# Performance work log

Measured on AMD Instinct MI355X. Metric: run time of the kernel, lower is better.

## Reference

```python
import jax, jax.numpy as jnp
import numpy as np

N, S, H = 16, 2048, 1024
K = 8           # num_models (experts)
D = H // 4      # bottleneck = hidden_dim // ds_factor


def setup_inputs() -> dict:
    key = jax.random.key(0)
    k1, k2, k3, k4, k5, k6 = jax.random.split(key, 6)
    hidden_states = jax.random.normal(k1, (N, S, H), dtype=jnp.float32)
    p = jax.random.uniform(k2, (N, K), dtype=jnp.float32)
    prob = p / jnp.sum(p, axis=-1, keepdims=True)  # normalized routing probs
    std = 0.02
    w_down = jax.random.normal(k3, (K, D, H), dtype=jnp.float32) * std
    b_down = jax.random.normal(k4, (K, D), dtype=jnp.float32) * std
    w_up = jax.random.normal(k5, (K, H, D), dtype=jnp.float32) * std
    b_up = jax.random.normal(k6, (K, H), dtype=jnp.float32) * std
    return {"hidden_states": hidden_states, "prob": prob,
            "w_down": w_down, "b_down": b_down,
            "w_up": w_up, "b_up": b_up}


def merge_linear(x, prob, weight, bias):
    # weight: (K, out, in); prob: (N, K) -> per-instance merged weight (N, out, in)
    w = jnp.einsum('nk,koi->noi', prob, weight)
    b = jnp.einsum('nk,ko->no', prob, bias)
    # x: (N, S, in) -> (N, S, out); matmul with per-instance weight^T
    y = jnp.einsum('nsi,noi->nso', x, w)
    return y + b[:, None, :]


def reference(hidden_states, prob, w_down, b_down, w_up, b_up):
    # MergeAdapter forward (ln_before=False, ln_after=False, dropout=0)
    residual = merge_linear(hidden_states, prob, w_down, b_down)
    residual = jax.nn.relu(residual)
    residual = merge_linear(residual, prob, w_up, b_up)
    return hidden_states + residual
```

## Files before the change

kernel.cpp:

```cpp
#include <hip/hip_runtime.h>


typedef unsigned short u16;
typedef __bf16 bf16x8 __attribute__((ext_vector_type(8)));
typedef float f32x4 __attribute__((ext_vector_type(4)));

__device__ __forceinline__ u16 f2bf(float f) {
    union { float f; unsigned int i; } v; v.f = f;
    unsigned int r = v.i + 0x7fffu + ((v.i >> 16) & 1u);
    return (u16)(r >> 16);
}

__device__ __forceinline__ void gload_lds16(const u16* g, u16* l) {
    __builtin_amdgcn_global_load_lds(
        (const __attribute__((address_space(1))) void*)g,
        (__attribute__((address_space(3))) void*)l,
        16, 0, 0);
}

__global__ __launch_bounds__(256)
void merge_kernel(const float* __restrict__ prob,
                  const float* __restrict__ w_down, const float* __restrict__ b_down,
                  const float* __restrict__ w_up,   const float* __restrict__ b_up,
                  u16* __restrict__ Wd, u16* __restrict__ Wu,
                  float* __restrict__ bd, float* __restrict__ bu)
{
    __shared__ float sp[128];
    const int tid = threadIdx.x;
    if (tid < 128) sp[tid] = prob[tid];
    __syncthreads();

    const int bid = blockIdx.x;
    const int E = 256 * 1024;

    if (bid < 256) {
        int v = bid * 256 + tid;
        const bool down = (v < 32768);
        const int vv = down ? v : (v - 32768);
        const float* W = down ? w_down : w_up;
        u16* O = down ? Wd : Wu;
        const size_t e = (size_t)vv * 8;

        float wf[8][8];
        #pragma unroll
        for (int k = 0; k < 8; ++k) {
            const float4 f0 = *(const float4*)(W + (size_t)k * E + e);
            const float4 f1 = *(const float4*)(W + (size_t)k * E + e + 4);
            wf[k][0] = f0.x; wf[k][1] = f0.y; wf[k][2] = f0.z; wf[k][3] = f0.w;
            wf[k][4] = f1.x; wf[k][5] = f1.y; wf[k][6] = f1.z; wf[k][7] = f1.w;
        }
        for (int n = 0; n < 16; ++n) {
            float a[8] = {0.f,0.f,0.f,0.f,0.f,0.f,0.f,0.f};
            #pragma unroll
            for (int k = 0; k < 8; ++k) {
                const float p = sp[n * 8 + k];
                #pragma unroll
                for (int j = 0; j < 8; ++j) a[j] = fmaf(p, wf[k][j], a[j]);
            }
            union { uint4 u; u16 s[8]; } ov;
            #pragma unroll
            for (int j = 0; j < 8; ++j) ov.s[j] = f2bf(a[j]);
            *(uint4*)(O + (size_t)n * E + e) = ov.u;
        }
    } else {
        int idx = (bid - 256) * 256 + tid;
        if (idx < 16 * 256) {
            const int n = idx >> 8, d = idx & 255;
            float s = 0.f;
            #pragma unroll
            for (int k = 0; k < 8; ++k)
                s = fmaf(sp[n * 8 + k], b_down[k * 256 + d], s);
            bd[idx] = s;
        } else {
            const int i2 = idx - 4096;
            const int n = i2 >> 10, h = i2 & 1023;
            float s = 0.f;
            #pragma unroll
            for (int k = 0; k < 8; ++k)
                s = fmaf(sp[n * 8 + k], b_up[k * 1024 + h], s);
            bu[i2] = s;
        }
    }
}

__global__ __launch_bounds__(256, 2)
void gemm_down(const float* __restrict__ A, const u16* __restrict__ B,
               const float* __restrict__ bias, u16* __restrict__ C,
               int M, int Nn, int K)
{
    __shared__ __align__(16) u16 As[128 * 64];
    __shared__ __align__(16) u16 Bs[128 * 64];

    const int batch = blockIdx.z;
    A += (size_t)batch * M * K;
    B += (size_t)batch * Nn * K;
    bias += (size_t)batch * Nn;
    C += (size_t)batch * M * Nn;

    const int tid = threadIdx.x;
    const int lane = tid & 63;
    const int wave = tid >> 6;
    const int wm = wave >> 1, wn = wave & 1;
    const int quad = lane >> 4, rl = lane & 15;
    const int tm = blockIdx.y, tn = blockIdx.x;

    const float* Ag = A + (size_t)tm * 128 * K;
    const u16* Bg = B + (size_t)tn * 128 * K;

    f32x4 acc[4][4] = {};

    for (int k0 = 0; k0 < K; k0 += 64) {
        #pragma unroll
        for (int r = 0; r < 4; ++r) {
            const int li = r * 256 + tid;
            const int row = li >> 3;
            const int col = (li & 7) * 8;
            const int ldsbase = (r * 256 + (tid & 192)) * 8;
            gload_lds16(Bg + (size_t)row * K + (k0 + col), &Bs[ldsbase]);
        }
        #pragma unroll
        for (int r = 0; r < 4; ++r) {
            const int li = r * 256 + tid;
            const int row = li >> 3;
            const int col = (li & 7) * 8;
            const float4 f0 = *(const float4*)(Ag + (size_t)row * K + (k0 + col));
            const float4 f1 = *(const float4*)(Ag + (size_t)row * K + (k0 + col) + 4);
            union { uint4 u; u16 s[8]; } cv;
            cv.s[0] = f2bf(f0.x); cv.s[1] = f2bf(f0.y);
            cv.s[2] = f2bf(f0.z); cv.s[3] = f2bf(f0.w);
            cv.s[4] = f2bf(f1.x); cv.s[5] = f2bf(f1.y);
            cv.s[6] = f2bf(f1.z); cv.s[7] = f2bf(f1.w);
            *(uint4*)(As + (size_t)li * 8) = cv.u;
        }
        __syncthreads();

        #pragma unroll
        for (int kk = 0; kk < 64; kk += 32) {
            bf16x8 af[4], bfr[4];
            #pragma unroll
            for (int mi = 0; mi < 4; ++mi)
                af[mi] = *(const bf16x8*)(As + (wm * 64 + mi * 16 + rl) * 64 + kk + quad * 8);
            #pragma unroll
            for (int ni = 0; ni < 4; ++ni)
                bfr[ni] = *(const bf16x8*)(Bs + (wn * 64 + ni * 16 + rl) * 64 + kk + quad * 8);
            #pragma unroll
            for (int mi = 0; mi < 4; ++mi)
                #pragma unroll
                for (int ni = 0; ni < 4; ++ni)
                    acc[mi][ni] = __builtin_amdgcn_mfma_f32_16x16x32_bf16(
                        af[mi], bfr[ni], acc[mi][ni], 0, 0, 0);
        }
        __syncthreads();
    }

    #pragma unroll
    for (int ni = 0; ni < 4; ++ni) {
        const int col = tn * 128 + wn * 64 + ni * 16 + rl;
        const float bv = bias[col];
        #pragma unroll
        for (int mi = 0; mi < 4; ++mi) {
            #pragma unroll
            for (int i = 0; i < 4; ++i) {
                const int row = tm * 128 + wm * 64 + mi * 16 + quad * 4 + i;
                float v = fmaxf(acc[mi][ni][i] + bv, 0.0f);
                C[(size_t)row * Nn + col] = f2bf(v);
            }
        }
    }
}

__global__ __launch_bounds__(256, 2)
void gemm_up(const u16* __restrict__ A, const u16* __restrict__ B,
             const float* __restrict__ bias, const float* __restrict__ Res,
             float* __restrict__ C, int M, int Nn, int K)
{
    __shared__ __align__(16) u16 As[128 * 64];
    __shared__ __align__(16) u16 Bs[128 * 64];

    const int batch = blockIdx.z;
    A += (size_t)batch * M * K;
    B += (size_t)batch * Nn * K;
    bias += (size_t)batch * Nn;
    Res += (size_t)batch * M * Nn;
    C += (size_t)batch * M * Nn;

    const int tid = threadIdx.x;
    const int lane = tid & 63;
    const int wave = tid >> 6;
    const int wm = wave >> 1, wn = wave & 1;
    const int quad = lane >> 4, rl = lane & 15;
    const int tm = blockIdx.y, tn = blockIdx.x;

    const u16* Ag = A + (size_t)tm * 128 * K;
    const u16* Bg = B + (size_t)tn * 128 * K;

    f32x4 acc[4][4] = {};

    for (int k0 = 0; k0 < K; k0 += 64) {
        #pragma unroll
        for (int r = 0; r < 4; ++r) {
            const int li = r * 256 + tid;
            const int row = li >> 3;
            const int col = (li & 7) * 8;
            const int ldsbase = (r * 256 + (tid & 192)) * 8;
            gload_lds16(Ag + (size_t)row * K + (k0 + col), &As[ldsbase]);
        }
        #pragma unroll
        for (int r = 0; r < 4; ++r) {
            const int li = r * 256 + tid;
            const int row = li >> 3;
            const int col = (li & 7) * 8;
            const int ldsbase = (r * 256 + (tid & 192)) * 8;
            gload_lds16(Bg + (size_t)row * K + (k0 + col), &Bs[ldsbase]);
        }
        __syncthreads();

        #pragma unroll
        for (int kk = 0; kk < 64; kk += 32) {
            bf16x8 af[4], bfr[4];
            #pragma unroll
            for (int mi = 0; mi < 4; ++mi)
                af[mi] = *(const bf16x8*)(As + (wm * 64 + mi * 16 + rl) * 64 + kk + quad * 8);
            #pragma unroll
            for (int ni = 0; ni < 4; ++ni)
                bfr[ni] = *(const bf16x8*)(Bs + (wn * 64 + ni * 16 + rl) * 64 + kk + quad * 8);
            #pragma unroll
            for (int mi = 0; mi < 4; ++mi)
                #pragma unroll
                for (int ni = 0; ni < 4; ++ni)
                    acc[mi][ni] = __builtin_amdgcn_mfma_f32_16x16x32_bf16(
                        af[mi], bfr[ni], acc[mi][ni], 0, 0, 0);
        }
        __syncthreads();
    }

    #pragma unroll
    for (int ni = 0; ni < 4; ++ni) {
        const int col = tn * 128 + wn * 64 + ni * 16 + rl;
        const float bv = bias[col];
        #pragma unroll
        for (int mi = 0; mi < 4; ++mi) {
            #pragma unroll
            for (int i = 0; i < 4; ++i) {
                const int row = tm * 128 + wm * 64 + mi * 16 + quad * 4 + i;
                const size_t off = (size_t)row * Nn + col;
                C[off] = acc[mi][ni][i] + bv + Res[off];
            }
        }
    }
}

extern "C" void kernel_launch(void* const* d_in, const int* in_sizes, int n_in,
                              void* d_out, int out_size, void* d_ws, size_t ws_size,
                              hipStream_t stream) {
    const float* hidden = (const float*)d_in[0];
    const float* prob   = (const float*)d_in[1];
    const float* w_down = (const float*)d_in[2];
    const float* b_down = (const float*)d_in[3];
    const float* w_up   = (const float*)d_in[4];
    const float* b_up   = (const float*)d_in[5];
    float* out = (float*)d_out;

    u16* Wd = (u16*)d_ws;
    u16* Wu = Wd + (size_t)16 * 256 * 1024;
    u16* R  = Wu + (size_t)16 * 1024 * 256;
    float* bd = (float*)(R + (size_t)16 * 2048 * 256);
    float* bu = bd + 16 * 256;

    merge_kernel<<<336, 256, 0, stream>>>(prob, w_down, b_down, w_up, b_up,
                                          Wd, Wu, bd, bu);

    gemm_down<<<dim3(2, 16, 16), 256, 0, stream>>>(
        hidden, Wd, bd, R, 2048, 256, 1024);

    gemm_up<<<dim3(8, 16, 16), 256, 0, stream>>>(
        R, Wu, bu, hidden, out, 2048, 1024, 256);
}
```

Baseline: 337.5 us.

## Fuse down and up projection GEMMs into one kernel with LDS-resident intermediate

Replaces the separate down-projection and up-projection GEMM kernels with one fused kernel. Each 512-thread block computes a 128-row tile of the ReLU bottleneck into LDS and then runs the up-projection over eight 128-column chunks, adding bias and the residual. This removes the global round trip of the intermediate activation and one launch. In exchange the grid shrinks to 256 large blocks at one block per CU, the up phase has no load/compute overlap, and x is read twice.

```diff
diff --git a/kernel.cpp b/kernel.cpp
--- a/kernel.cpp
+++ b/kernel.cpp
@@ -83,168 +83,135 @@
     }
 }
 
-__global__ __launch_bounds__(256, 2)
-void gemm_down(const float* __restrict__ A, const u16* __restrict__ B,
-               const float* __restrict__ bias, u16* __restrict__ C,
-               int M, int Nn, int K)
+__global__ __launch_bounds__(512, 1)
+void fused_adapter(const float* __restrict__ x, const u16* __restrict__ Wd,
+                   const u16* __restrict__ Wu, const float* __restrict__ bd,
+                   const float* __restrict__ bu, float* __restrict__ out)
 {
-    __shared__ __align__(16) u16 As[128 * 64];
-    __shared__ __align__(16) u16 Bs[128 * 64];
-
-    const int batch = blockIdx.z;
-    A += (size_t)batch * M * K;
-    B += (size_t)batch * Nn * K;
-    bias += (size_t)batch * Nn;
-    C += (size_t)batch * M * Nn;
-
-    const int tid = threadIdx.x;
+    __shared__ __align__(16) u16 Rs[128 * 256];
+    __shared__ __align__(16) u16 stage[32768];
+
+    const int tid  = threadIdx.x;
     const int lane = tid & 63;
     const int wave = tid >> 6;
-    const int wm = wave >> 1, wn = wave & 1;
     const int quad = lane >> 4, rl = lane & 15;
-    const int tm = blockIdx.y, tn = blockIdx.x;
-
-    const float* Ag = A + (size_t)tm * 128 * K;
-    const u16* Bg = B + (size_t)tn * 128 * K;
-
-    f32x4 acc[4][4] = {};
-
-    for (int k0 = 0; k0 < K; k0 += 64) {
-        #pragma unroll
-        for (int r = 0; r < 4; ++r) {
-            const int li = r * 256 + tid;
-            const int row = li >> 3;
-            const int col = (li & 7) * 8;
-            const int ldsbase = (r * 256 + (tid & 192)) * 8;
-            gload_lds16(Bg + (size_t)row * K + (k0 + col), &Bs[ldsbase]);
-        }
-        #pragma unroll
-        for (int r = 0; r < 4; ++r) {
-            const int li = r * 256 + tid;
-            const int row = li >> 3;
-            const int col = (li & 7) * 8;
-            const float4 f0 = *(const float4*)(Ag + (size_t)row * K + (k0 + col));
-            const float4 f1 = *(const float4*)(Ag + (size_t)row * K + (k0 + col) + 4);
+
+    const int id = blockIdx.x;
+    const int r4 = id & 15;
+    const int batch = (r4 & 7) * 2 + (r4 >> 3);
+    const int mblk  = id >> 4;
+
+    const float* xb  = x  + (size_t)batch * 2048 * 1024 + (size_t)mblk * 128 * 1024;
+    const u16*   Wdb = Wd + (size_t)batch * 256 * 1024;
+    const u16*   Wub = Wu + (size_t)batch * 1024 * 256;
+    const float* bdb = bd + batch * 256;
+    const float* bub = bu + batch * 1024;
+    float*       ob  = out + (size_t)batch * 2048 * 1024 + (size_t)mblk * 128 * 1024;
+
+    u16* xs  = stage;
+    u16* wds = stage + 8192;
+
+    const int wm1 = wave >> 2, wn1 = wave & 3;
+    f32x4 acc1[4][4] = {};
+
+    for (int k0 = 0; k0 < 1024; k0 += 64) {
+        #pragma unroll
+        for (int rr = 0; rr < 4; ++rr) {
+            const int li  = rr * 512 + tid;
+            const int row = li >> 3, col = (li & 7) * 8;
+            gload_lds16(Wdb + (size_t)row * 1024 + (k0 + col),
+                        wds + (size_t)(rr * 512 + wave * 64) * 8);
+        }
+        #pragma unroll
+        for (int rr = 0; rr < 2; ++rr) {
+            const int li  = rr * 512 + tid;
+            const int row = li >> 3, col = (li & 7) * 8;
+            const float4 f0 = *(const float4*)(xb + (size_t)row * 1024 + (k0 + col));
+            const float4 f1 = *(const float4*)(xb + (size_t)row * 1024 + (k0 + col) + 4);
             union { uint4 u; u16 s[8]; } cv;
-            cv.s[0] = f2bf(f0.x); cv.s[1] = f2bf(f0.y);
-            cv.s[2] = f2bf(f0.z); cv.s[3] = f2bf(f0.w);
-            cv.s[4] = f2bf(f1.x); cv.s[5] = f2bf(f1.y);
-            cv.s[6] = f2bf(f1.z); cv.s[7] = f2bf(f1.w);
-            *(uint4*)(As + (size_t)li * 8) = cv.u;
+            cv.s[0]=f2bf(f0.x); cv.s[1]=f2bf(f0.y); cv.s[2]=f2bf(f0.z); cv.s[3]=f2bf(f0.w);
+            cv.s[4]=f2bf(f1.x); cv.s[5]=f2bf(f1.y); cv.s[6]=f2bf(f1.z); cv.s[7]=f2bf(f1.w);
+            *(uint4*)(xs + (size_t)li * 8) = cv.u;
         }
         __syncthreads();
 
         #pragma unroll
         for (int kk = 0; kk < 64; kk += 32) {
-            bf16x8 af[4], bfr[4];
-            #pragma unroll
-            for (int mi = 0; mi < 4; ++mi)
-                af[mi] = *(const bf16x8*)(As + (wm * 64 + mi * 16 + rl) * 64 + kk + quad * 8);
+            bf16x8 af[4], bfv[4];
+            #pragma unroll
+            for (int mi = 0; mi < 4; ++mi)
+                af[mi] = *(const bf16x8*)(xs + (wm1 * 64 + mi * 16 + rl) * 64 + kk + quad * 8);
             #pragma unroll
             for (int ni = 0; ni < 4; ++ni)
-                bfr[ni] = *(const bf16x8*)(Bs + (wn * 64 + ni * 16 + rl) * 64 + kk + quad * 8);
+                bfv[ni] = *(const bf16x8*)(wds + (wn1 * 64 + ni * 16 + rl) * 64 + kk + quad * 8);
             #pragma unroll
             for (int mi = 0; mi < 4; ++mi)
                 #pragma unroll
                 for (int ni = 0; ni < 4; ++ni)
-                    acc[mi][ni] = __builtin_amdgcn_mfma_f32_16x16x32_bf16(
-                        af[mi], bfr[ni], acc[mi][ni], 0, 0, 0);
+                    acc1[mi][ni] = __builtin_amdgcn_mfma_f32_16x16x32_bf16(
+                        af[mi], bfv[ni], acc1[mi][ni], 0, 0, 0);
         }
         __syncthreads();
     }
 
     #pragma unroll
     for (int ni = 0; ni < 4; ++ni) {
-        const int col = tn * 128 + wn * 64 + ni * 16 + rl;
-        const float bv = bias[col];
+        const int col = wn1 * 64 + ni * 16 + rl;
+        const float bv = bdb[col];
         #pragma unroll
         for (int mi = 0; mi < 4; ++mi) {
             #pragma unroll
             for (int i = 0; i < 4; ++i) {
-                const int row = tm * 128 + wm * 64 + mi * 16 + quad * 4 + i;
-                float v = fmaxf(acc[mi][ni][i] + bv, 0.0f);
-                C[(size_t)row * Nn + col] = f2bf(v);
+                const int row = wm1 * 64 + mi * 16 + quad * 4 + i;
+                Rs[row * 256 + col] = f2bf(fmaxf(acc1[mi][ni][i] + bv, 0.0f));
             }
         }
     }
-}
-
-__global__ __launch_bounds__(256, 2)
-void gemm_up(const u16* __restrict__ A, const u16* __restrict__ B,
-             const float* __restrict__ bias, const float* __restrict__ Res,
-             float* __restrict__ C, int M, int Nn, int K)
-{
-    __shared__ __align__(16) u16 As[128 * 64];
-    __shared__ __align__(16) u16 Bs[128 * 64];
-
-    const int batch = blockIdx.z;
-    A += (size_t)batch * M * K;
-    B += (size_t)batch * Nn * K;
-    bias += (size_t)batch * Nn;
-    Res += (size_t)batch * M * Nn;
-    C += (size_t)batch * M * Nn;
-
-    const int tid = threadIdx.x;
-    const int lane = tid & 63;
-    const int wave = tid >> 6;
-    const int wm = wave >> 1, wn = wave & 1;
-    const int quad = lane >> 4, rl = lane & 15;
-    const int tm = blockIdx.y, tn = blockIdx.x;
-
-    const u16* Ag = A + (size_t)tm * 128 * K;
-    const u16* Bg = B + (size_t)tn * 128 * K;
-
-    f32x4 acc[4][4] = {};
-
-    for (int k0 = 0; k0 < K; k0 += 64) {
-        #pragma unroll
-        for (int r = 0; r < 4; ++r) {
-            const int li = r * 256 + tid;
-            const int row = li >> 3;
-            const int col = (li & 7) * 8;
-            const int ldsbase = (r * 256 + (tid & 192)) * 8;
-            gload_lds16(Ag + (size_t)row * K + (k0 + col), &As[ldsbase]);
-        }
-        #pragma unroll
-        for (int r = 0; r < 4; ++r) {
-            const int li = r * 256 + tid;
-            const int row = li >> 3;
-            const int col = (li & 7) * 8;
-            const int ldsbase = (r * 256 + (tid & 192)) * 8;
-            gload_lds16(Bg + (size_t)row * K + (k0 + col), &Bs[ldsbase]);
-        }
-        __syncthreads();
-
-        #pragma unroll
-        for (int kk = 0; kk < 64; kk += 32) {
-            bf16x8 af[4], bfr[4];
-            #pragma unroll
-            for (int mi = 0; mi < 4; ++mi)
-                af[mi] = *(const bf16x8*)(As + (wm * 64 + mi * 16 + rl) * 64 + kk + quad * 8);
-            #pragma unroll
-            for (int ni = 0; ni < 4; ++ni)
-                bfr[ni] = *(const bf16x8*)(Bs + (wn * 64 + ni * 16 + rl) * 64 + kk + quad * 8);
-            #pragma unroll
-            for (int mi = 0; mi < 4; ++mi)
-                #pragma unroll
-                for (int ni = 0; ni < 4; ++ni)
-                    acc[mi][ni] = __builtin_amdgcn_mfma_f32_16x16x32_bf16(
-                        af[mi], bfr[ni], acc[mi][ni], 0, 0, 0);
-        }
-        __syncthreads();
-    }
-
-    #pragma unroll
-    for (int ni = 0; ni < 4; ++ni) {
-        const int col = tn * 128 + wn * 64 + ni * 16 + rl;
-        const float bv = bias[col];
-        #pragma unroll
-        for (int mi = 0; mi < 4; ++mi) {
-            #pragma unroll
-            for (int i = 0; i < 4; ++i) {
-                const int row = tm * 128 + wm * 64 + mi * 16 + quad * 4 + i;
-                const size_t off = (size_t)row * Nn + col;
-                C[off] = acc[mi][ni][i] + bv + Res[off];
+
+    const int wm2 = wave >> 2, wn2 = wave & 3;
+
+    for (int c = 0; c < 8; ++c) {
+        __syncthreads();
+
+        #pragma unroll
+        for (int rr = 0; rr < 8; ++rr) {
+            const int li  = rr * 512 + tid;
+            const int row = li >> 5, col = (li & 31) * 8;
+            gload_lds16(Wub + (size_t)(c * 128 + row) * 256 + col,
+                        stage + (size_t)(rr * 512 + wave * 64) * 8);
+        }
+        __syncthreads();
+
+        f32x4 acc2[4][2] = {};
+        #pragma unroll
+        for (int kk = 0; kk < 256; kk += 32) {
+            bf16x8 af[4], bfv[2];
+            #pragma unroll
+            for (int mi = 0; mi < 4; ++mi)
+                af[mi] = *(const bf16x8*)(Rs + (wm2 * 64 + mi * 16 + rl) * 256 + kk + quad * 8);
+            #pragma unroll
+            for (int ni = 0; ni < 2; ++ni)
+                bfv[ni] = *(const bf16x8*)(stage + (wn2 * 32 + ni * 16 + rl) * 256 + kk + quad * 8);
+            #pragma unroll
+            for (int mi = 0; mi < 4; ++mi)
+                #pragma unroll
+                for (int ni = 0; ni < 2; ++ni)
+                    acc2[mi][ni] = __builtin_amdgcn_mfma_f32_16x16x32_bf16(
+                        af[mi], bfv[ni], acc2[mi][ni], 0, 0, 0);
+        }
+
+        #pragma unroll
+        for (int ni = 0; ni < 2; ++ni) {
+            const int colg = c * 128 + wn2 * 32 + ni * 16 + rl;
+            const float bv = bub[colg];
+            #pragma unroll
+            for (int mi = 0; mi < 4; ++mi) {
+                #pragma unroll
+                for (int i = 0; i < 4; ++i) {
+                    const int rowl = wm2 * 64 + mi * 16 + quad * 4 + i;
+                    const size_t off = (size_t)rowl * 1024 + colg;
+                    ob[off] = acc2[mi][ni][i] + bv + xb[off];
+                }
             }
         }
     }
@@ -263,16 +230,11 @@
 
     u16* Wd = (u16*)d_ws;
     u16* Wu = Wd + (size_t)16 * 256 * 1024;
-    u16* R  = Wu + (size_t)16 * 1024 * 256;
-    float* bd = (float*)(R + (size_t)16 * 2048 * 256);
+    float* bd = (float*)(Wu + (size_t)16 * 1024 * 256);
     float* bu = bd + 16 * 256;
 
     merge_kernel<<<336, 256, 0, stream>>>(prob, w_down, b_down, w_up, b_up,
                                           Wd, Wu, bd, bu);
 
-    gemm_down<<<dim3(2, 16, 16), 256, 0, stream>>>(
-        hidden, Wd, bd, R, 2048, 256, 1024);
-
-    gemm_up<<<dim3(8, 16, 16), 256, 0, stream>>>(
-        R, Wu, bu, hidden, out, 2048, 1024, 256);
-}
+    fused_adapter<<<256, 512, 0, stream>>>(hidden, Wd, Wu, bd, bu, out);
+}
```

Measured after the change: 331.7 us. No clear change (-1.7%).
